# Performance work log

Measured on AMD Instinct MI355X. Metric: run time of the kernel, lower is better.

The kernel has to match this reference:

```python
import jax, jax.numpy as jnp
import numpy as np


def setup_inputs() -> dict:
    key = jax.random.key(0)
    ks = jax.random.split(key, 6)
    B, C, H, W = 2, 256, 128, 512
    img1 = jax.random.normal(ks[0], (B, C, H, W), jnp.float32)
    img2 = jax.random.normal(ks[1], (B, C, H, W), jnp.float32)
    intri1 = jax.random.uniform(ks[2], (B, 3, 3), jnp.float32)
    intri2 = jax.random.uniform(ks[3], (B, 3, 3), jnp.float32)
    extri1 = jax.random.uniform(ks[4], (B, 4, 4), jnp.float32)
    extri2 = jax.random.uniform(ks[5], (B, 4, 4), jnp.float32)
    return {"img1": img1, "img2": img2, "intri1": intri1, "intri2": intri2,
            "extri1": extri1, "extri2": extri2}


TEMPERATURE = 1.0  # init default
DISP_CLAMP = 0.1   # from corresp_prob_to_depth_conf


def reference(img1, img2, intri1, intri2, extri1, extri2):
    """CostVolume(dot, dual=False, pack_lr=False, geometry_mask=True).forward.
    Returns (depth, confidence), each (B, 1, H, W). G=1 group dim kept.
    """
    B, C, H, W = img1.shape
    # full per-row correlation volume: vol[b,h,w1,w2] = <img1[:,w1], img2[:,w2]> / sqrt(C)
    vol = jnp.einsum('bchw,bchv->bhwv', img1, img2) / jnp.asarray(np.sqrt(C), img1.dtype)
    idx = jnp.arange(W, dtype=vol.dtype)
    # left_first=True -> lower-triangular geometry mask (correspondence w2 <= w1)
    tril = (idx[None, :] <= idx[:, None]).astype(vol.dtype)  # (W1, W2)
    # NOTE: mask is applied AFTER softmax (prob is NOT renormalized), as in source
    prob = jax.nn.softmax(vol / TEMPERATURE, axis=-1) * tril  # (B,H,W1,W2)
    corresp = jnp.sum(prob * idx, axis=-1)[:, None]  # soft-argmax index, (B,1,H,W)
    confidence = jnp.max(prob, axis=-1)[:, None]      # (B,1,H,W)
    # corresp2disp with normalize=True (normalized_intri default True)
    disp = jnp.abs(corresp - idx) / W
    disp = jnp.clip(disp, DISP_CLAMP)
    # d2d_transform (reconstructed): pinhole disparity->depth, depth = fx * baseline / disp
    fx = intri1[:, 0, 0][:, None, None, None]
    baseline = jnp.linalg.norm(extri1[:, :3, 3] - extri2[:, :3, 3], axis=-1)[:, None, None, None]
    depth = fx * baseline / disp
    return depth, confidence
```

## Files before the change

### kernel.cpp

```cpp
#include <hip/hip_runtime.h>
#include <hip/hip_bf16.h>

typedef __attribute__((ext_vector_type(4))) float f32x4;
typedef __attribute__((ext_vector_type(8))) short s16x8;

#define C_DIM 256
#define H_DIM 128
#define W_DIM 512
#define HW    (H_DIM * W_DIM)
#define CHW   (C_DIM * HW)
#define WS_NEED (2ull * 128 * 512 * 256 * 2)

__device__ __forceinline__ unsigned short f2bf(float f) {
    return __builtin_bit_cast(unsigned short, __float2bfloat16(f));
}

__device__ __forceinline__ void gl_lds16(const void* g, void* l) {
    __builtin_amdgcn_global_load_lds(
        (const __attribute__((address_space(1))) void*)g,
        (__attribute__((address_space(3))) void*)l, 16, 0, 0);
}

__global__ __launch_bounds__(256) void transpose_kernel(
    const float* __restrict__ img2, unsigned short* __restrict__ bws)
{
    __shared__ unsigned short tile[64][65];
    const int t = threadIdx.x;
    const int d = blockIdx.x;
    const int cb = d & 3, wb = (d >> 2) & 7, bh = d >> 5;
    const int b = bh >> 7, h = bh & 127;
    const float* src = img2 + (size_t)b * CHW + (size_t)h * W_DIM
                            + (size_t)(cb * 64) * HW + wb * 64;
    {
        const int c = t >> 2, w0 = (t & 3) << 4;
        const float* p = src + (size_t)c * HW + w0;
        #pragma unroll
        for (int i = 0; i < 16; i += 4) {
            f32x4 v = *(const f32x4*)(p + i);
            #pragma unroll
            for (int j = 0; j < 4; ++j) tile[c][w0 + i + j] = f2bf(v[j]);
        }
    }
    __syncthreads();
    {
        const int n_l = t >> 2, c4 = (t & 3) << 4;
        unsigned short vals[16];
        #pragma unroll
        for (int i = 0; i < 16; ++i) vals[i] = tile[c4 + i][n_l];
        unsigned short* dst = bws + ((size_t)bh * 512 + wb * 64 + n_l) * 256 + cb * 64 + c4;
        *(s16x8*)(dst)     = *(s16x8*)&vals[0];
        *(s16x8*)(dst + 8) = *(s16x8*)&vals[8];
    }
}

__global__ __launch_bounds__(512, 4) void costvol_kernel(
    const float* __restrict__ img1, const unsigned short* __restrict__ bws,
    const float* __restrict__ intri1,
    const float* __restrict__ extri1, const float* __restrict__ extri2,
    float* __restrict__ out)
{
    __shared__ __align__(16) unsigned char smem[65536];
    unsigned short* Alds = (unsigned short*)smem;

    const int t = threadIdx.x;
    const int d = blockIdx.x;
    const int win = d >> 6, pos = d & 63;
    const int bh    = win * 8 + (pos & 7);
    const int w1blk = pos >> 3;
    const int b = bh >> 7, h = bh & 127;
    const int w1base = w1blk * 64;

    const int wv = t >> 6, lane = t & 63;
    const int lrow = lane & 15, hq = lane >> 4;

    const unsigned short* bsrc0 =
        bws + ((size_t)bh * 512 + 64 * wv + (lane >> 2)) * 256
            + 8 * ((lane & 3) ^ ((lane >> 3) & 3));
    unsigned char* const bdst = smem + 32768 + wv * 4096;

    #pragma unroll
    for (int i = 0; i < 4; ++i)
        gl_lds16(bsrc0 + i * 4096, bdst + i * 1024);

    const float* i1 = img1 + (size_t)b * CHW + (size_t)h * W_DIM;
    {
        const int c    = t >> 1;
        const int wseg = (t & 1) << 5;
        const float* src = i1 + (size_t)c * HW + (size_t)(w1base + wseg);
        #pragma unroll
        for (int i0 = 0; i0 < 32; i0 += 4) {
            f32x4 v = *(const f32x4*)(src + i0);
            #pragma unroll
            for (int j = 0; j < 4; ++j) {
                const int w = wseg + i0 + j;
                Alds[w * 256 + ((((c >> 3) ^ (w & 15)) << 3) | (c & 7))] = f2bf(v[j] * 0.0625f);
            }
        }
    }
    __syncthreads();

    f32x4 acc[4][4] = {};

    int boff[4];
    #pragma unroll
    for (int w2t = 0; w2t < 4; ++w2t)
        boff[w2t] = (16 * w2t + lrow) * 64 + 16 * (hq ^ ((lrow >> 1) & 3));

    #pragma unroll
    for (int kc = 0; kc < 8; ++kc) {
        s16x8 bfr[4], afr[4];
        #pragma unroll
        for (int w2t = 0; w2t < 4; ++w2t)
            bfr[w2t] = *(const s16x8*)(bdst + boff[w2t]);
        #pragma unroll
        for (int w1t = 0; w1t < 4; ++w1t) {
            const int row = 16 * w1t + lrow;
            const int kb  = (kc << 2) + hq;
            afr[w1t] = *(const s16x8*)&Alds[row * 256 + ((kb ^ (row & 15)) << 3)];
        }
        asm volatile("s_waitcnt lgkmcnt(0)" ::: "memory");
        __builtin_amdgcn_sched_barrier(0);
        if (kc < 7) {
            #pragma unroll
            for (int i = 0; i < 4; ++i)
                gl_lds16(bsrc0 + (kc + 1) * 32 + i * 4096, bdst + i * 1024);
        }
        __builtin_amdgcn_sched_barrier(0);
        #pragma unroll
        for (int w2t = 0; w2t < 4; ++w2t)
            #pragma unroll
            for (int w1t = 0; w1t < 4; ++w1t)
                acc[w2t][w1t] = __builtin_amdgcn_mfma_f32_16x16x32_bf16(
                    bfr[w2t], afr[w1t], acc[w2t][w1t], 0, 0, 0);
        if (kc < 7)
            asm volatile("s_waitcnt vmcnt(0)" ::: "memory");
    }

    __syncthreads();

    float (*red)[64][3] = (float(*)[64][3])smem;
    #pragma unroll
    for (int w1t = 0; w1t < 4; ++w1t) {
        const int w1l = 16 * w1t + lrow;
        const int w1g = w1base + w1l;
        float Se = 0.f, Sei = 0.f, Me = 0.f;
        #pragma unroll
        for (int w2t = 0; w2t < 4; ++w2t) {
            #pragma unroll
            for (int r = 0; r < 4; ++r) {
                const int w2 = 64 * wv + 16 * w2t + 4 * hq + r;
                const float e = __expf(acc[w2t][w1t][r]);
                Se += e;
                if (w2 <= w1g) { Sei += e * (float)w2; Me = fmaxf(Me, e); }
            }
        }
        Se  += __shfl_xor(Se, 16, 64);  Se  += __shfl_xor(Se, 32, 64);
        Sei += __shfl_xor(Sei, 16, 64); Sei += __shfl_xor(Sei, 32, 64);
        Me = fmaxf(Me, __shfl_xor(Me, 16, 64)); Me = fmaxf(Me, __shfl_xor(Me, 32, 64));
        if (hq == 0) {
            red[wv][w1l][0] = Se;
            red[wv][w1l][1] = Sei;
            red[wv][w1l][2] = Me;
        }
    }
    __syncthreads();

    if (t < 64) {
        const int row = t;
        float Se = 0.f, Sei = 0.f, Me = 0.f;
        #pragma unroll
        for (int q = 0; q < 8; ++q) {
            Se  += red[q][row][0];
            Sei += red[q][row][1];
            Me   = fmaxf(Me, red[q][row][2]);
        }
        const int w1g = w1base + row;
        const float corresp = Sei / Se;
        const float conf    = Me / Se;
        float disp = fabsf(corresp - (float)w1g) * (1.0f / 512.0f);
        disp = fmaxf(disp, 0.1f);
        const float fx = intri1[b * 9];
        const float dx = extri1[b * 16 + 3]  - extri2[b * 16 + 3];
        const float dy = extri1[b * 16 + 7]  - extri2[b * 16 + 7];
        const float dz = extri1[b * 16 + 11] - extri2[b * 16 + 11];
        const float bl = sqrtf(dx * dx + dy * dy + dz * dz);
        const float depth = fx * bl / disp;
        const int oidx = b * HW + h * W_DIM + w1g;
        out[oidx]          = depth;
        out[2 * HW + oidx] = conf;
    }
}

__global__ __launch_bounds__(512, 4) void costvol_fallback(
    const float* __restrict__ img1, const float* __restrict__ img2,
    const float* __restrict__ intri1,
    const float* __restrict__ extri1, const float* __restrict__ extri2,
    float* __restrict__ out)
{
    __shared__ __align__(16) unsigned char smem[32768];
    unsigned short* Alds = (unsigned short*)smem;
    const int t = threadIdx.x;
    const int d = blockIdx.x;
    const int win = d >> 6, pos = d & 63;
    const int bh    = win * 8 + (pos & 7);
    const int w1blk = pos >> 3;
    const int b = bh >> 7, h = bh & 127;
    const int w1base = w1blk * 64;
    const float* i1 = img1 + (size_t)b * CHW + (size_t)h * W_DIM;
    const float* i2 = img2 + (size_t)b * CHW + (size_t)h * W_DIM;
    {
        const int c    = t >> 1;
        const int wseg = (t & 1) << 5;
        const float* src = i1 + (size_t)c * HW + (size_t)(w1base + wseg);
        #pragma unroll
        for (int i0 = 0; i0 < 32; i0 += 4) {
            f32x4 v = *(const f32x4*)(src + i0);
            #pragma unroll
            for (int j = 0; j < 4; ++j) {
                const int w = wseg + i0 + j;
                Alds[w * 256 + ((((c >> 3) ^ (w & 15)) << 3) | (c & 7))] = f2bf(v[j]);
            }
        }
    }
    __syncthreads();
    const int wn = t >> 6, lane = t & 63;
    const int lrow = lane & 15, hq = lane >> 4;
    const float* pb[4];
    #pragma unroll
    for (int ct = 0; ct < 4; ++ct)
        pb[ct] = i2 + (size_t)(8 * hq) * HW + (64 * wn + 16 * ct + lrow);
    f32x4 acc[4][4] = {};
    for (int kc = 0; kc < 8; ++kc) {
        s16x8 afr[4];
        #pragma unroll
        for (int rt = 0; rt < 4; ++rt) {
            const int row = 16 * rt + lrow;
            const int kb  = (kc << 2) + hq;
            afr[rt] = *(const s16x8*)&Alds[row * 256 + ((kb ^ (row & 15)) << 3)];
        }
        #pragma unroll
        for (int ct = 0; ct < 4; ++ct) {
            const float* p = pb[ct] + (size_t)(32 * kc) * HW;
            float f[8];
            #pragma unroll
            for (int j = 0; j < 8; ++j) f[j] = p[(size_t)j * HW];
            s16x8 bfr;
            #pragma unroll
            for (int j = 0; j < 8; ++j) bfr[j] = (short)f2bf(f[j]);
            #pragma unroll
            for (int rt = 0; rt < 4; ++rt)
                acc[rt][ct] = __builtin_amdgcn_mfma_f32_16x16x32_bf16(afr[rt], bfr, acc[rt][ct], 0, 0, 0);
        }
    }
    __syncthreads();
    float (*red)[64][3] = (float(*)[64][3])smem;
    #pragma unroll
    for (int rt = 0; rt < 4; ++rt) {
        #pragma unroll
        for (int r = 0; r < 4; ++r) {
            const int row = 16 * rt + 4 * hq + r;
            const int w1g = w1base + row;
            float Se = 0.f, Sei = 0.f, Me = 0.f;
            #pragma unroll
            for (int ct = 0; ct < 4; ++ct) {
                const int col = 64 * wn + 16 * ct + lrow;
                const float e = __expf(acc[rt][ct][r] * 0.0625f);
                Se += e;
                if (col <= w1g) { Sei += e * (float)col; Me = fmaxf(Me, e); }
            }
            #pragma unroll
            for (int m = 1; m < 16; m <<= 1) {
                Se  += __shfl_xor(Se,  m, 64);
                Sei += __shfl_xor(Sei, m, 64);
                Me   = fmaxf(Me, __shfl_xor(Me, m, 64));
            }
            if (lrow == 0) { red[wn][row][0] = Se; red[wn][row][1] = Sei; red[wn][row][2] = Me; }
        }
    }
    __syncthreads();
    if (t < 64) {
        const int row = t;
        float Se = 0.f, Sei = 0.f, Me = 0.f;
        #pragma unroll
        for (int q = 0; q < 8; ++q) {
            Se += red[q][row][0]; Sei += red[q][row][1]; Me = fmaxf(Me, red[q][row][2]);
        }
        const int w1g = w1base + row;
        const float corresp = Sei / Se;
        const float conf    = Me / Se;
        float disp = fabsf(corresp - (float)w1g) * (1.0f / 512.0f);
        disp = fmaxf(disp, 0.1f);
        const float fx = intri1[b * 9];
        const float dx = extri1[b * 16 + 3]  - extri2[b * 16 + 3];
        const float dy = extri1[b * 16 + 7]  - extri2[b * 16 + 7];
        const float dz = extri1[b * 16 + 11] - extri2[b * 16 + 11];
        const float bl = sqrtf(dx * dx + dy * dy + dz * dz);
        const int oidx = b * HW + h * W_DIM + w1g;
        out[oidx]          = fx * bl / disp;
        out[2 * HW + oidx] = conf;
    }
}

extern "C" void kernel_launch(void* const* d_in, const int* in_sizes, int n_in,
                              void* d_out, int out_size, void* d_ws, size_t ws_size,
                              hipStream_t stream) {
    const float* img1   = (const float*)d_in[0];
    const float* img2   = (const float*)d_in[1];
    const float* intri1 = (const float*)d_in[2];
    const float* extri1 = (const float*)d_in[4];
    const float* extri2 = (const float*)d_in[5];
    if (ws_size >= WS_NEED) {
        unsigned short* bws = (unsigned short*)d_ws;
        transpose_kernel<<<dim3(8192), dim3(256), 0, stream>>>(img2, bws);
        costvol_kernel<<<dim3(2048), dim3(512), 0, stream>>>(
            img1, bws, intri1, extri1, extri2, (float*)d_out);
    } else {
        costvol_fallback<<<dim3(2048), dim3(512), 0, stream>>>(
            img1, img2, intri1, extri1, extri2, (float*)d_out);
    }
}
```

Measured before the change: 122.8 us.

## Halve w1 tile and read B fragments directly from global instead of LDS staging

The cost-volume kernel now handles 32 w1 columns per block instead of 64, which doubles the grid to 4096 blocks and shrinks shared memory from 64KB to 16KB so more blocks can be resident. The global_load_lds pipeline that staged img2 (B) tiles through LDS is removed. Each lane now loads its B fragments straight from the transposed bf16 workspace in global memory. This drops the staging waits and LDS traffic, but B data is re-read from global or cache twice as often, and each thread does fewer MFMAs per B fragment.

New measurement: 179.9 us. +46.5%, slower.

```diff
diff --git a/kernel.cpp b/kernel.cpp
--- a/kernel.cpp
+++ b/kernel.cpp
@@ -13,12 +13,6 @@
 
 __device__ __forceinline__ unsigned short f2bf(float f) {
     return __builtin_bit_cast(unsigned short, __float2bfloat16(f));
-}
-
-__device__ __forceinline__ void gl_lds16(const void* g, void* l) {
-    __builtin_amdgcn_global_load_lds(
-        (const __attribute__((address_space(1))) void*)g,
-        (__attribute__((address_space(3))) void*)l, 16, 0, 0);
 }
 
 __global__ __launch_bounds__(256) void transpose_kernel(
@@ -59,88 +53,70 @@
     const float* __restrict__ extri1, const float* __restrict__ extri2,
     float* __restrict__ out)
 {
-    __shared__ __align__(16) unsigned char smem[65536];
+    __shared__ __align__(16) unsigned char smem[16384];
     unsigned short* Alds = (unsigned short*)smem;
 
     const int t = threadIdx.x;
     const int d = blockIdx.x;
-    const int win = d >> 6, pos = d & 63;
-    const int bh    = win * 8 + (pos & 7);
+    const int pos = d & 127;
+    const int bh    = (d >> 7) * 8 + (pos & 7);
     const int w1blk = pos >> 3;
     const int b = bh >> 7, h = bh & 127;
-    const int w1base = w1blk * 64;
+    const int w1base = w1blk * 32;
 
     const int wv = t >> 6, lane = t & 63;
     const int lrow = lane & 15, hq = lane >> 4;
 
-    const unsigned short* bsrc0 =
-        bws + ((size_t)bh * 512 + 64 * wv + (lane >> 2)) * 256
-            + 8 * ((lane & 3) ^ ((lane >> 3) & 3));
-    unsigned char* const bdst = smem + 32768 + wv * 4096;
-
-    #pragma unroll
-    for (int i = 0; i < 4; ++i)
-        gl_lds16(bsrc0 + i * 4096, bdst + i * 1024);
-
     const float* i1 = img1 + (size_t)b * CHW + (size_t)h * W_DIM;
     {
-        const int c    = t >> 1;
-        const int wseg = (t & 1) << 5;
-        const float* src = i1 + (size_t)c * HW + (size_t)(w1base + wseg);
-        #pragma unroll
-        for (int i0 = 0; i0 < 32; i0 += 4) {
+        const int c  = t >> 1;
+        const int w0 = (t & 1) << 4;
+        const float* src = i1 + (size_t)c * HW + (size_t)(w1base + w0);
+        #pragma unroll
+        for (int i0 = 0; i0 < 16; i0 += 4) {
             f32x4 v = *(const f32x4*)(src + i0);
             #pragma unroll
             for (int j = 0; j < 4; ++j) {
-                const int w = wseg + i0 + j;
+                const int w = w0 + i0 + j;
                 Alds[w * 256 + ((((c >> 3) ^ (w & 15)) << 3) | (c & 7))] = f2bf(v[j] * 0.0625f);
             }
         }
     }
     __syncthreads();
 
-    f32x4 acc[4][4] = {};
-
-    int boff[4];
+    const unsigned short* pb[4];
     #pragma unroll
     for (int w2t = 0; w2t < 4; ++w2t)
-        boff[w2t] = (16 * w2t + lrow) * 64 + 16 * (hq ^ ((lrow >> 1) & 3));
+        pb[w2t] = bws + ((size_t)bh * 512 + 64 * wv + 16 * w2t + lrow) * 256 + 8 * hq;
+
+    f32x4 acc[4][2] = {};
 
     #pragma unroll
     for (int kc = 0; kc < 8; ++kc) {
-        s16x8 bfr[4], afr[4];
+        s16x8 bfr[4];
         #pragma unroll
         for (int w2t = 0; w2t < 4; ++w2t)
-            bfr[w2t] = *(const s16x8*)(bdst + boff[w2t]);
-        #pragma unroll
-        for (int w1t = 0; w1t < 4; ++w1t) {
+            bfr[w2t] = *(const s16x8*)(pb[w2t] + (kc << 5));
+        s16x8 afr[2];
+        #pragma unroll
+        for (int w1t = 0; w1t < 2; ++w1t) {
             const int row = 16 * w1t + lrow;
             const int kb  = (kc << 2) + hq;
             afr[w1t] = *(const s16x8*)&Alds[row * 256 + ((kb ^ (row & 15)) << 3)];
         }
-        asm volatile("s_waitcnt lgkmcnt(0)" ::: "memory");
-        __builtin_amdgcn_sched_barrier(0);
-        if (kc < 7) {
-            #pragma unroll
-            for (int i = 0; i < 4; ++i)
-                gl_lds16(bsrc0 + (kc + 1) * 32 + i * 4096, bdst + i * 1024);
-        }
-        __builtin_amdgcn_sched_barrier(0);
         #pragma unroll
         for (int w2t = 0; w2t < 4; ++w2t)
             #pragma unroll
-            for (int w1t = 0; w1t < 4; ++w1t)
+            for (int w1t = 0; w1t < 2; ++w1t)
                 acc[w2t][w1t] = __builtin_amdgcn_mfma_f32_16x16x32_bf16(
                     bfr[w2t], afr[w1t], acc[w2t][w1t], 0, 0, 0);
-        if (kc < 7)
-            asm volatile("s_waitcnt vmcnt(0)" ::: "memory");
-    }
-
-    __syncthreads();
-
-    float (*red)[64][3] = (float(*)[64][3])smem;
-    #pragma unroll
-    for (int w1t = 0; w1t < 4; ++w1t) {
+    }
+
+    __syncthreads();
+
+    float (*red)[32][3] = (float(*)[32][3])smem;
+    #pragma unroll
+    for (int w1t = 0; w1t < 2; ++w1t) {
         const int w1l = 16 * w1t + lrow;
         const int w1g = w1base + w1l;
         float Se = 0.f, Sei = 0.f, Me = 0.f;
@@ -165,7 +141,7 @@
     }
     __syncthreads();
 
-    if (t < 64) {
+    if (t < 32) {
         const int row = t;
         float Se = 0.f, Sei = 0.f, Me = 0.f;
         #pragma unroll
@@ -312,7 +288,7 @@
     if (ws_size >= WS_NEED) {
         unsigned short* bws = (unsigned short*)d_ws;
         transpose_kernel<<<dim3(8192), dim3(256), 0, stream>>>(img2, bws);
-        costvol_kernel<<<dim3(2048), dim3(512), 0, stream>>>(
+        costvol_kernel<<<dim3(4096), dim3(512), 0, stream>>>(
             img1, bws, intri1, extri1, extri2, (float*)d_out);
     } else {
         costvol_fallback<<<dim3(2048), dim3(512), 0, stream>>>(
```

## Triple-buffer per-wave B tiles in LDS to overlap global loads with MFMA

Applied to the files above, without the earlier changes.

Each wave now streams its img2 (B) slice through a three-slot ring of 16-element K sub-chunks in LDS, prefetching two sub-chunks ahead, instead of a single buffer refilled per K step. The waitcnt now allows outstanding loads (vmcnt(2)) rather than draining to zero after every step, so global-to-LDS traffic is meant to overlap with the MFMA work. This grows shared memory from 64KB to 80KB per block, which may reduce occupancy. It also adds more complex swizzle and wrap-around indexing, which carries some correctness risk.

Result: slower. 137.5 us (+12.0%).

```diff
diff --git a/kernel.cpp b/kernel.cpp
--- a/kernel.cpp
+++ b/kernel.cpp
@@ -59,7 +59,7 @@
     const float* __restrict__ extri1, const float* __restrict__ extri2,
     float* __restrict__ out)
 {
-    __shared__ __align__(16) unsigned char smem[65536];
+    __shared__ __align__(16) unsigned char smem[81920];
     unsigned short* Alds = (unsigned short*)smem;
 
     const int t = threadIdx.x;
@@ -72,15 +72,23 @@
 
     const int wv = t >> 6, lane = t & 63;
     const int lrow = lane & 15, hq = lane >> 4;
-
-    const unsigned short* bsrc0 =
-        bws + ((size_t)bh * 512 + 64 * wv + (lane >> 2)) * 256
-            + 8 * ((lane & 3) ^ ((lane >> 3) & 3));
-    unsigned char* const bdst = smem + 32768 + wv * 4096;
-
-    #pragma unroll
-    for (int i = 0; i < 4; ++i)
-        gl_lds16(bsrc0 + i * 4096, bdst + i * 1024);
+    const int hqhi = hq >> 1;
+
+    unsigned char* const Bwave = smem + 32768 + wv * 6144;
+    const unsigned short* bsrc[2];
+    #pragma unroll
+    for (int i = 0; i < 2; ++i) {
+        const int u   = i * 64 + lane;
+        const int row = u >> 1;
+        const int k8e = (u & 1) ^ ((u >> 3) & 1);
+        bsrc[i] = bws + ((size_t)bh * 512 + 64 * wv + row) * 256 + 8 * k8e;
+    }
+
+    #pragma unroll
+    for (int s = 0; s < 3; ++s)
+        #pragma unroll
+        for (int i = 0; i < 2; ++i)
+            gl_lds16(bsrc[i] + s * 16, Bwave + s * 2048 + i * 1024);
 
     const float* i1 = img1 + (size_t)b * CHW + (size_t)h * W_DIM;
     {
@@ -103,15 +111,29 @@
 
     int boff[4];
     #pragma unroll
-    for (int w2t = 0; w2t < 4; ++w2t)
-        boff[w2t] = (16 * w2t + lrow) * 64 + 16 * (hq ^ ((lrow >> 1) & 3));
+    for (int w2t = 0; w2t < 4; ++w2t) {
+        const int row = 16 * w2t + lrow;
+        boff[w2t] = row * 32 + (((hq & 1) ^ ((row >> 2) & 1)) << 4) + hqhi * 2048;
+    }
+    const int wrapfix = hqhi ? -6144 : 0;
 
     #pragma unroll
     for (int kc = 0; kc < 8; ++kc) {
+        if (kc < 7)
+            asm volatile("s_waitcnt vmcnt(2)" ::: "memory");
+        else
+            asm volatile("s_waitcnt vmcnt(0)" ::: "memory");
+        __builtin_amdgcn_sched_barrier(0);
+
+        const int c3   = (2 * kc) % 3;
+        const int base = c3 * 2048 + ((c3 == 2) ? 0 : 0);
         s16x8 bfr[4], afr[4];
         #pragma unroll
-        for (int w2t = 0; w2t < 4; ++w2t)
-            bfr[w2t] = *(const s16x8*)(bdst + boff[w2t]);
+        for (int w2t = 0; w2t < 4; ++w2t) {
+            int off = base + boff[w2t];
+            if (c3 == 2) off += wrapfix;
+            bfr[w2t] = *(const s16x8*)(Bwave + off);
+        }
         #pragma unroll
         for (int w1t = 0; w1t < 4; ++w1t) {
             const int row = 16 * w1t + lrow;
@@ -120,10 +142,14 @@
         }
         asm volatile("s_waitcnt lgkmcnt(0)" ::: "memory");
         __builtin_amdgcn_sched_barrier(0);
-        if (kc < 7) {
-            #pragma unroll
-            for (int i = 0; i < 4; ++i)
-                gl_lds16(bsrc0 + (kc + 1) * 32 + i * 4096, bdst + i * 1024);
+        #pragma unroll
+        for (int q = 0; q < 2; ++q) {
+            const int s = 2 * kc + 3 + q;
+            if (s < 16) {
+                #pragma unroll
+                for (int i = 0; i < 2; ++i)
+                    gl_lds16(bsrc[i] + s * 16, Bwave + (s % 3) * 2048 + i * 1024);
+            }
         }
         __builtin_amdgcn_sched_barrier(0);
         #pragma unroll
@@ -132,8 +158,6 @@
             for (int w1t = 0; w1t < 4; ++w1t)
                 acc[w2t][w1t] = __builtin_amdgcn_mfma_f32_16x16x32_bf16(
                     bfr[w2t], afr[w1t], acc[w2t][w1t], 0, 0, 0);
-        if (kc < 7)
-            asm volatile("s_waitcnt vmcnt(0)" ::: "memory");
     }
 
     __syncthreads();
```
